# Kernel optimization log

Measured on AMD Instinct MI355X. Metric: run time of the kernel, lower is better.

The kernel has to match this reference:

```python
import jax, jax.numpy as jnp
import numpy as np

N_NODES = 100000
N_EDGES = 1600000
IN_DIM = 128
OUT_DIM = 64


def setup_inputs() -> dict:
    key = jax.random.key(0)
    k1, k2, k3, k4 = jax.random.split(key, 4)
    h = jax.random.normal(k1, (N_NODES, IN_DIM), dtype=jnp.float32)
    W = jax.random.normal(k2, (OUT_DIM, IN_DIM), dtype=jnp.float32) * (1.0 / np.sqrt(IN_DIM))
    a_w = jax.random.normal(k3, (1, 2 * OUT_DIM), dtype=jnp.float32) * (1.0 / np.sqrt(2 * OUT_DIM))
    edge_index = jax.random.randint(k4, (2, N_EDGES), 0, N_NODES, dtype=jnp.int64 if jax.config.jax_enable_x64 else jnp.int32)
    return {"h": h, "W": W, "a_w": a_w, "edge_index": edge_index}


def reference(h, W, a_w, edge_index):
    # Wh: [N, out_dim]  (Linear without bias: x @ W.T)
    Wh = h @ W.T
    src, dst = edge_index[0], edge_index[1]
    # per-edge concat [Wh[src], Wh[dst]] -> [E, 2*out_dim]
    e = jnp.concatenate([Wh[src], Wh[dst]], axis=-1)
    # attention logits: [E]
    alpha = jax.nn.leaky_relu(e @ a_w.T, negative_slope=0.2)[:, 0]
    # global-max-stabilized exp (matches the torch code exactly)
    alpha_exp = jnp.exp(alpha - jnp.max(alpha))
    # segment softmax denominator over destination nodes: [N]
    alpha_sum = jax.ops.segment_sum(alpha_exp, dst, num_segments=N_NODES)
    alpha_norm = alpha_exp / (alpha_sum[dst] + 1e-9)
    # weighted scatter-add aggregation: [N, out_dim]
    out = jax.ops.segment_sum(alpha_norm[:, None] * Wh[src], dst, num_segments=N_NODES)
    return (jax.nn.elu(out), alpha_norm)
```

## Files before the change

### kernel.cpp

```cpp
#include <hip/hip_runtime.h>
#include <math.h>

#define N_NODES 100000
#define N_EDGES 1600000
#define IN_DIM 128
#define OUT_DIM 64

#define BSHIFT 9
#define BSIZE  (1 << BSHIFT)
#define NB     ((N_NODES + BSIZE - 1) >> BSHIFT)
#define EDGES_PER_BLK 4096
#define NBLK   ((N_EDGES + EDGES_PER_BLK - 1) / EDGES_PER_BLK)
#define SCANA_LEN (NB * NBLK)
#define SCANA_ITEMS 1024
#define SCANA_NB ((SCANA_LEN + SCANA_ITEMS - 1) / SCANA_ITEMS)

typedef short short8 __attribute__((ext_vector_type(8)));
typedef float f32x4 __attribute__((ext_vector_type(4)));
typedef float f32x2 __attribute__((ext_vector_type(2)));

__device__ __forceinline__ unsigned short f2bf(float x) {
    unsigned int u = __float_as_uint(x);
    return (unsigned short)((u + 0x7FFFu + ((u >> 16) & 1u)) >> 16);
}
__device__ __forceinline__ short8 pack_bf16x8(float4 p, float4 q) {
    short8 r;
    r[0] = (short)f2bf(p.x); r[1] = (short)f2bf(p.y);
    r[2] = (short)f2bf(p.z); r[3] = (short)f2bf(p.w);
    r[4] = (short)f2bf(q.x); r[5] = (short)f2bf(q.y);
    r[6] = (short)f2bf(q.z); r[7] = (short)f2bf(q.w);
    return r;
}
__device__ __forceinline__ void pk_fma(f32x2& d, f32x2 a, f32x2 b) {
    asm("v_pk_fma_f32 %0, %1, %2, %0" : "+v"(d) : "v"(a), "v"(b));
}

__global__ __launch_bounds__(256) void k_histA(const int* __restrict__ dst,
                                               int* __restrict__ hist_t,
                                               const float* __restrict__ W,
                                               const float* __restrict__ a_w,
                                               float* __restrict__ w1,
                                               float* __restrict__ w2) {
    __shared__ int lhist[NB];
    const int tid = threadIdx.x;
    const int blk = blockIdx.x;
    if (blk == 0 && tid < IN_DIM) {
        float r1 = 0.f, r2 = 0.f;
        #pragma unroll 8
        for (int dd = 0; dd < OUT_DIM; ++dd) {
            float wv = W[dd * IN_DIM + tid];
            r1 = fmaf(a_w[dd], wv, r1);
            r2 = fmaf(a_w[OUT_DIM + dd], wv, r2);
        }
        w1[tid] = r1; w2[tid] = r2;
    }
    if (tid < NB) lhist[tid] = 0;
    __syncthreads();
    const int e0 = blk * EDGES_PER_BLK;
    #pragma unroll
    for (int j = 0; j < 4; ++j) {
        int e = e0 + (j * 256 + tid) * 4;
        if (e >= N_EDGES) continue;
        int4 d4 = *(const int4*)(dst + e);
        atomicAdd(&lhist[d4.x >> BSHIFT], 1);
        atomicAdd(&lhist[d4.y >> BSHIFT], 1);
        atomicAdd(&lhist[d4.z >> BSHIFT], 1);
        atomicAdd(&lhist[d4.w >> BSHIFT], 1);
    }
    __syncthreads();
    if (tid < NB) hist_t[tid * NBLK + blk] = lhist[tid];
}

__global__ __launch_bounds__(256) void k_wh(const float* __restrict__ h,
                                            const float* __restrict__ W,
                                            const float* __restrict__ w1,
                                            const float* __restrict__ w2,
                                            unsigned short* __restrict__ Wh16,
                                            float* __restrict__ s1,
                                            float* __restrict__ s2) {
    const int tid = threadIdx.x;
    const int wv = tid >> 6;
    const int l  = tid & 63;
    const int g  = l >> 4;
    const int lm = l & 15;
    const int node0 = blockIdx.x * 64 + wv * 16;
    const int row = node0 + lm;
    const int rowc = (row < N_NODES) ? row : (N_NODES - 1);
    const float* hrow = h + (size_t)rowc * IN_DIM;

    short8 afrag[4];
    float sp1 = 0.f, sp2 = 0.f;
    #pragma unroll
    for (int kt = 0; kt < 4; ++kt) {
        const int k0 = kt * 32 + g * 8;
        float4 p = *(const float4*)(hrow + k0);
        float4 q = *(const float4*)(hrow + k0 + 4);
        float4 u1 = *(const float4*)(w1 + k0);
        float4 v1 = *(const float4*)(w1 + k0 + 4);
        float4 u2 = *(const float4*)(w2 + k0);
        float4 v2 = *(const float4*)(w2 + k0 + 4);
        sp1 += p.x*u1.x + p.y*u1.y + p.z*u1.z + p.w*u1.w
             + q.x*v1.x + q.y*v1.y + q.z*v1.z + q.w*v1.w;
        sp2 += p.x*u2.x + p.y*u2.y + p.z*u2.z + p.w*u2.w
             + q.x*v2.x + q.y*v2.y + q.z*v2.z + q.w*v2.w;
        afrag[kt] = pack_bf16x8(p, q);
    }
    sp1 += __shfl_xor(sp1, 16, 64); sp1 += __shfl_xor(sp1, 32, 64);
    sp2 += __shfl_xor(sp2, 16, 64); sp2 += __shfl_xor(sp2, 32, 64);
    if (l < 16 && row < N_NODES) { s1[row] = sp1; s2[row] = sp2; }

    f32x4 acc[4] = {f32x4{0,0,0,0}, f32x4{0,0,0,0}, f32x4{0,0,0,0}, f32x4{0,0,0,0}};
    #pragma unroll
    for (int nt = 0; nt < 4; ++nt) {
        #pragma unroll
        for (int kt = 0; kt < 4; ++kt) {
            const float* wr = W + (size_t)(nt * 16 + lm) * IN_DIM + kt * 32 + g * 8;
            float4 p = *(const float4*)wr;
            float4 q = *(const float4*)(wr + 4);
            short8 bfrag = pack_bf16x8(p, q);
            acc[nt] = __builtin_amdgcn_mfma_f32_16x16x32_bf16(afrag[kt], bfrag, acc[nt], 0, 0, 0);
        }
    }
    #pragma unroll
    for (int nt = 0; nt < 4; ++nt) {
        #pragma unroll
        for (int r = 0; r < 4; ++r) {
            int nodo = node0 + g * 4 + r;
            if (nodo < N_NODES)
                Wh16[(size_t)nodo * OUT_DIM + nt * 16 + lm] = f2bf(acc[nt][r]);
        }
    }
}

__global__ __launch_bounds__(256) void k_scanA_part(const int* __restrict__ in,
                                                    int* __restrict__ bsum) {
    __shared__ int wsum[4];
    const int tid = threadIdx.x;
    const int base = blockIdx.x * SCANA_ITEMS + tid * 4;
    int s = 0;
    #pragma unroll
    for (int j = 0; j < 4; ++j) {
        int i = base + j;
        if (i < SCANA_LEN) s += in[i];
    }
    #pragma unroll
    for (int off = 32; off > 0; off >>= 1) s += __shfl_xor(s, off, 64);
    if ((tid & 63) == 0) wsum[tid >> 6] = s;
    __syncthreads();
    if (tid == 0) bsum[blockIdx.x] = wsum[0] + wsum[1] + wsum[2] + wsum[3];
}

__global__ __launch_bounds__(128) void k_scanA_mid(int* __restrict__ bsum) {
    __shared__ int s[128];
    const int tid = threadIdx.x;
    s[tid] = (tid < SCANA_NB) ? bsum[tid] : 0;
    __syncthreads();
    #pragma unroll
    for (int off = 1; off < 128; off <<= 1) {
        int u = (tid >= off) ? s[tid - off] : 0;
        __syncthreads();
        s[tid] += u;
        __syncthreads();
    }
    if (tid < SCANA_NB) bsum[tid] = (tid > 0) ? s[tid - 1] : 0;
}

__global__ __launch_bounds__(256) void k_scanA_final(const int* __restrict__ in,
                                                     const int* __restrict__ bsum,
                                                     int* __restrict__ outscan) {
    __shared__ int wtot[4];
    const int tid = threadIdx.x;
    const int lane = tid & 63;
    const int wid = tid >> 6;
    const int base = blockIdx.x * SCANA_ITEMS + tid * 4;
    int c[4];
    #pragma unroll
    for (int j = 0; j < 4; ++j)
        c[j] = (base + j < SCANA_LEN) ? in[base + j] : 0;
    int tot = c[0] + c[1] + c[2] + c[3];
    int inc = tot;
    #pragma unroll
    for (int off = 1; off < 64; off <<= 1) {
        int u = __shfl_up(inc, off, 64);
        if (lane >= off) inc += u;
    }
    if (lane == 63) wtot[wid] = inc;
    __syncthreads();
    int wbase = 0;
    #pragma unroll
    for (int w = 0; w < 4; ++w) wbase += (w < wid) ? wtot[w] : 0;
    int run = bsum[blockIdx.x] + wbase + (inc - tot);
    #pragma unroll
    for (int j = 0; j < 4; ++j) {
        int i = base + j;
        if (i < SCANA_LEN) { outscan[i] = run; run += c[j]; }
    }
}

__global__ __launch_bounds__(256) void k_binA(const int* __restrict__ ei,
                                              const float* __restrict__ s1,
                                              const float* __restrict__ s2,
                                              const int* __restrict__ flat_scan,
                                              int2* __restrict__ brec,
                                              float* __restrict__ ae_orig) {
    __shared__ int lbase[NB];
    __shared__ int lcur[NB];
    const int tid = threadIdx.x;
    const int blk = blockIdx.x;
    if (tid < NB) { lbase[tid] = flat_scan[tid * NBLK + blk]; lcur[tid] = 0; }
    __syncthreads();
    const int e0 = blk * EDGES_PER_BLK;
    #pragma unroll
    for (int j = 0; j < 4; ++j) {
        int e = e0 + (j * 256 + tid) * 4;
        if (e >= N_EDGES) continue;
        int4 s4 = *(const int4*)(ei + e);
        int4 d4 = *(const int4*)(ei + N_EDGES + e);
        float4 aev;
        #pragma unroll
        for (int q = 0; q < 4; ++q) {
            int src = ((const int*)&s4)[q];
            int dst = ((const int*)&d4)[q];
            float a = s1[src] + s2[dst];
            a = (a > 0.f) ? a : 0.2f * a;
            float ae = expf(a);
            ((float*)&aev)[q] = ae;
            int b = dst >> BSHIFT;
            int r = atomicAdd(&lcur[b], 1);
            brec[lbase[b] + r] = make_int2(src | ((dst & (BSIZE - 1)) << 17),
                                           __float_as_int(ae));
        }
        *(float4*)(ae_orig + e) = aev;
    }
}

__global__ __launch_bounds__(256) void k_fine(const int2* __restrict__ brec,
                                              const int* __restrict__ flat_scan,
                                              int* __restrict__ offsets,
                                              int2* __restrict__ sa_sorted,
                                              float* __restrict__ inv_tab) {
    __shared__ int lhist[BSIZE];
    __shared__ int lofs[BSIZE];
    __shared__ int lcur[BSIZE];
    __shared__ float lsum[BSIZE];
    __shared__ int wsum[4];
    const int tid = threadIdx.x;
    const int lane = tid & 63;
    const int wid = tid >> 6;
    const int b = blockIdx.x;
    const int base = flat_scan[b * NBLK];
    const int endp = (b + 1 < NB) ? flat_scan[(b + 1) * NBLK] : N_EDGES;
    const int cnt = endp - base;
    lhist[tid] = 0; lhist[tid + 256] = 0;
    lsum[tid] = 0.f; lsum[tid + 256] = 0.f;
    __syncthreads();
    for (int i = tid; i < cnt; i += 256)
        atomicAdd(&lhist[(unsigned)brec[base + i].x >> 17], 1);
    __syncthreads();
    int c0 = lhist[2 * tid], c1 = lhist[2 * tid + 1];
    int s = c0 + c1;
    int inc = s;
    #pragma unroll
    for (int off = 1; off < 64; off <<= 1) {
        int u = __shfl_up(inc, off, 64);
        if (lane >= off) inc += u;
    }
    if (lane == 63) wsum[wid] = inc;
    __syncthreads();
    int wb = 0;
    #pragma unroll
    for (int w = 0; w < 4; ++w) wb += (w < wid) ? wsum[w] : 0;
    int ex = wb + inc - s;
    lofs[2 * tid] = ex; lofs[2 * tid + 1] = ex + c0;
    lcur[2 * tid] = ex; lcur[2 * tid + 1] = ex + c0;
    __syncthreads();
    const int dst0 = b << BSHIFT;
    #pragma unroll
    for (int j = 0; j < 2; ++j) {
        int jj = tid + j * 256;
        int node = dst0 + jj;
        if (node < N_NODES) offsets[node] = base + lofs[jj];
    }
    if (b == NB - 1 && tid == 0) offsets[N_NODES] = N_EDGES;
    for (int i = tid; i < cnt; i += 256) {
        int2 rec = brec[base + i];
        int dstl = (unsigned)rec.x >> 17;
        float ae = __int_as_float(rec.y);
        int pos = base + atomicAdd(&lcur[dstl], 1);
        sa_sorted[pos] = make_int2(rec.x & 0x1FFFF, rec.y);
        atomicAdd(&lsum[dstl], ae);
    }
    __syncthreads();
    #pragma unroll
    for (int j = 0; j < 2; ++j) {
        int jj = tid + j * 256;
        int node = dst0 + jj;
        if (node < N_NODES) inv_tab[node] = 1.f / (lsum[jj] + 1e-9f);
    }
}

__global__ __launch_bounds__(256) void k_agg(const int2* __restrict__ sa_sorted,
                                             const int* __restrict__ offsets,
                                             const unsigned short* __restrict__ Wh16,
                                             const float* __restrict__ inv_tab,
                                             float* __restrict__ out) {
    const int gid = blockIdx.x * 256 + threadIdx.x;
    const int node = gid >> 6;
    const int l = gid & 63;
    if (node >= N_NODES) return;
    const int g = l >> 3;
    const int o = l & 7;
    const int beg = offsets[node];
    const int end = offsets[node + 1];
    f32x2 acc2[4] = {f32x2{0,0}, f32x2{0,0}, f32x2{0,0}, f32x2{0,0}};
    int i = beg;
    for (; i + 16 <= end; i += 16) {
        int2 pA = sa_sorted[i + g];
        int2 pB = sa_sorted[i + 8 + g];
        const int4 rA = *(const int4*)(Wh16 + ((size_t)pA.x << 6) + (o << 3));
        const int4 rB = *(const int4*)(Wh16 + ((size_t)pB.x << 6) + (o << 3));
        float aeA = __int_as_float(pA.y);
        float aeB = __int_as_float(pB.y);
        f32x2 a2A = {aeA, aeA}, a2B = {aeB, aeB};
        #pragma unroll
        for (int q = 0; q < 4; ++q) {
            int v = ((const int*)&rA)[q];
            f32x2 f = { __uint_as_float((unsigned)v << 16),
                        __uint_as_float((unsigned)v & 0xFFFF0000u) };
            pk_fma(acc2[q], f, a2A);
        }
        #pragma unroll
        for (int q = 0; q < 4; ++q) {
            int v = ((const int*)&rB)[q];
            f32x2 f = { __uint_as_float((unsigned)v << 16),
                        __uint_as_float((unsigned)v & 0xFFFF0000u) };
            pk_fma(acc2[q], f, a2B);
        }
    }
    for (; i < end; i += 8) {
        int idx = i + g;
        int2 p = (idx < end) ? sa_sorted[idx] : make_int2(0, 0);
        const int4 r = *(const int4*)(Wh16 + ((size_t)p.x << 6) + (o << 3));
        float ae = __int_as_float(p.y);
        f32x2 a2 = {ae, ae};
        #pragma unroll
        for (int q = 0; q < 4; ++q) {
            int v = ((const int*)&r)[q];
            f32x2 f = { __uint_as_float((unsigned)v << 16),
                        __uint_as_float((unsigned)v & 0xFFFF0000u) };
            pk_fma(acc2[q], f, a2);
        }
    }
    #pragma unroll
    for (int m = 8; m <= 32; m <<= 1) {
        #pragma unroll
        for (int q = 0; q < 4; ++q) {
            acc2[q].x += __shfl_xor(acc2[q].x, m, 64);
            acc2[q].y += __shfl_xor(acc2[q].y, m, 64);
        }
    }
    if (g == 0) {
        const float inv = inv_tab[node];
        float e[8];
        #pragma unroll
        for (int q = 0; q < 4; ++q) {
            float x0 = acc2[q].x * inv;
            float x1 = acc2[q].y * inv;
            e[2*q]   = (x0 > 0.f) ? x0 : expf(x0) - 1.f;
            e[2*q+1] = (x1 > 0.f) ? x1 : expf(x1) - 1.f;
        }
        float* orow = out + (size_t)node * OUT_DIM + o * 8;
        *(float4*)orow = make_float4(e[0], e[1], e[2], e[3]);
        *(float4*)(orow + 4) = make_float4(e[4], e[5], e[6], e[7]);
    }
}

__global__ __launch_bounds__(256) void k_norm(const int* __restrict__ dst_arr,
                                              const float* __restrict__ ae_orig,
                                              const float* __restrict__ inv_tab,
                                              float* __restrict__ alpha_norm) {
    int t = blockIdx.x * 256 + threadIdx.x;
    if (t >= N_EDGES / 4) return;
    int4 d4 = ((const int4*)dst_arr)[t];
    float4 a4 = ((const float4*)ae_orig)[t];
    float4 r;
    r.x = a4.x * inv_tab[d4.x];
    r.y = a4.y * inv_tab[d4.y];
    r.z = a4.z * inv_tab[d4.z];
    r.w = a4.w * inv_tab[d4.w];
    ((float4*)alpha_norm)[t] = r;
}

extern "C" void kernel_launch(void* const* d_in, const int* in_sizes, int n_in,
                              void* d_out, int out_size, void* d_ws, size_t ws_size,
                              hipStream_t stream) {
    const float* h   = (const float*)d_in[0];
    const float* W   = (const float*)d_in[1];
    const float* a_w = (const float*)d_in[2];
    const int*   ei  = (const int*)d_in[3];

    float* out        = (float*)d_out;
    float* alpha_norm = out + (size_t)N_NODES * OUT_DIM;

    char* ws = (char*)d_ws;
    int2* brec      = (int2*)ws;            ws += (size_t)N_EDGES * 8;
    int2* sa_sorted = (int2*)ws;            ws += (size_t)N_EDGES * 8;
    unsigned short* Wh16 = (unsigned short*)ws;  ws += (size_t)N_NODES * OUT_DIM * 2;
    float* ae_orig  = (float*)ws;           ws += (size_t)N_EDGES * 4;
    float* s1       = (float*)ws;           ws += (size_t)N_NODES * 4;
    float* s2       = (float*)ws;           ws += (size_t)N_NODES * 4;
    int*   hist_t   = (int*)ws;             ws += (size_t)SCANA_LEN * 4;
    int*   flat_scan= (int*)ws;             ws += (size_t)SCANA_LEN * 4;
    int*   bsum     = (int*)ws;             ws += (size_t)SCANA_NB * 4;
    int*   offsets  = (int*)ws;             ws += (size_t)(N_NODES + 1) * 4;
    float* inv_tab  = (float*)ws;           ws += (size_t)N_NODES * 4;
    float* w1       = (float*)ws;           ws += (size_t)IN_DIM * 4;
    float* w2       = (float*)ws;           ws += (size_t)IN_DIM * 4;

    k_histA<<<NBLK, 256, 0, stream>>>(ei + N_EDGES, hist_t, W, a_w, w1, w2);
    k_wh<<<(N_NODES + 63) / 64, 256, 0, stream>>>(h, W, w1, w2, Wh16, s1, s2);
    k_scanA_part<<<SCANA_NB, 256, 0, stream>>>(hist_t, bsum);
    k_scanA_mid<<<1, 128, 0, stream>>>(bsum);
    k_scanA_final<<<SCANA_NB, 256, 0, stream>>>(hist_t, bsum, flat_scan);
    k_binA<<<NBLK, 256, 0, stream>>>(ei, s1, s2, flat_scan, brec, ae_orig);
    k_fine<<<NB, 256, 0, stream>>>(brec, flat_scan, offsets, sa_sorted, inv_tab);
    k_agg<<<(N_NODES * 64 + 255) / 256, 256, 0, stream>>>(sa_sorted, offsets, Wh16,
                                                          inv_tab, out);
    k_norm<<<(N_EDGES / 4 + 255) / 256, 256, 0, stream>>>(ei + N_EDGES, ae_orig,
                                                          inv_tab, alpha_norm);
}
```

Measured before the change: 165.2 us.

## Shrink edge blocks, fold mid scan into final, widen fine kernel, add nontemporal access

Edge blocks for histogram and binning now cover 1024 edges, which gives more workgroups. The scan uses 2048 items per block, and each final-scan block rescans the block partial sums, which removes the separate mid-scan launch. The fine sort kernel runs with 1024 threads per block, and streaming loads and stores use nontemporal hints. Smaller edge blocks make the histogram table and scan four times larger. The redundant per-block scan also adds barrier work.

```diff
diff --git a/kernel.cpp b/kernel.cpp
--- a/kernel.cpp
+++ b/kernel.cpp
@@ -9,15 +9,17 @@
 #define BSHIFT 9
 #define BSIZE  (1 << BSHIFT)
 #define NB     ((N_NODES + BSIZE - 1) >> BSHIFT)
-#define EDGES_PER_BLK 4096
+#define EDGES_PER_BLK 1024
 #define NBLK   ((N_EDGES + EDGES_PER_BLK - 1) / EDGES_PER_BLK)
 #define SCANA_LEN (NB * NBLK)
-#define SCANA_ITEMS 1024
+#define SCANA_ITEMS 2048
 #define SCANA_NB ((SCANA_LEN + SCANA_ITEMS - 1) / SCANA_ITEMS)
 
 typedef short short8 __attribute__((ext_vector_type(8)));
 typedef float f32x4 __attribute__((ext_vector_type(4)));
 typedef float f32x2 __attribute__((ext_vector_type(2)));
+typedef int   i32x2 __attribute__((ext_vector_type(2)));
+typedef int   i32x4 __attribute__((ext_vector_type(4)));
 
 __device__ __forceinline__ unsigned short f2bf(float x) {
     unsigned int u = __float_as_uint(x);
@@ -56,11 +58,8 @@
     }
     if (tid < NB) lhist[tid] = 0;
     __syncthreads();
-    const int e0 = blk * EDGES_PER_BLK;
-    #pragma unroll
-    for (int j = 0; j < 4; ++j) {
-        int e = e0 + (j * 256 + tid) * 4;
-        if (e >= N_EDGES) continue;
+    const int e = blk * EDGES_PER_BLK + tid * 4;
+    if (e < N_EDGES) {
         int4 d4 = *(const int4*)(dst + e);
         atomicAdd(&lhist[d4.x >> BSHIFT], 1);
         atomicAdd(&lhist[d4.y >> BSHIFT], 1);
@@ -136,48 +135,56 @@
                                                     int* __restrict__ bsum) {
     __shared__ int wsum[4];
     const int tid = threadIdx.x;
-    const int base = blockIdx.x * SCANA_ITEMS + tid * 4;
+    const int base = blockIdx.x * SCANA_ITEMS + tid * 8;
     int s = 0;
-    #pragma unroll
-    for (int j = 0; j < 4; ++j) {
-        int i = base + j;
-        if (i < SCANA_LEN) s += in[i];
+    if (base + 7 < SCANA_LEN) {
+        int4 a = *(const int4*)(in + base);
+        int4 b = *(const int4*)(in + base + 4);
+        s = a.x + a.y + a.z + a.w + b.x + b.y + b.z + b.w;
+    } else {
+        for (int j = 0; j < 8; ++j)
+            if (base + j < SCANA_LEN) s += in[base + j];
     }
     #pragma unroll
     for (int off = 32; off > 0; off >>= 1) s += __shfl_xor(s, off, 64);
     if ((tid & 63) == 0) wsum[tid >> 6] = s;
     __syncthreads();
     if (tid == 0) bsum[blockIdx.x] = wsum[0] + wsum[1] + wsum[2] + wsum[3];
-}
-
-__global__ __launch_bounds__(128) void k_scanA_mid(int* __restrict__ bsum) {
-    __shared__ int s[128];
-    const int tid = threadIdx.x;
-    s[tid] = (tid < SCANA_NB) ? bsum[tid] : 0;
-    __syncthreads();
-    #pragma unroll
-    for (int off = 1; off < 128; off <<= 1) {
-        int u = (tid >= off) ? s[tid - off] : 0;
-        __syncthreads();
-        s[tid] += u;
-        __syncthreads();
-    }
-    if (tid < SCANA_NB) bsum[tid] = (tid > 0) ? s[tid - 1] : 0;
 }
 
 __global__ __launch_bounds__(256) void k_scanA_final(const int* __restrict__ in,
                                                      const int* __restrict__ bsum,
                                                      int* __restrict__ outscan) {
+    __shared__ int sb[256];
     __shared__ int wtot[4];
     const int tid = threadIdx.x;
     const int lane = tid & 63;
     const int wid = tid >> 6;
-    const int base = blockIdx.x * SCANA_ITEMS + tid * 4;
-    int c[4];
-    #pragma unroll
-    for (int j = 0; j < 4; ++j)
-        c[j] = (base + j < SCANA_LEN) ? in[base + j] : 0;
-    int tot = c[0] + c[1] + c[2] + c[3];
+    sb[tid] = (tid < SCANA_NB) ? bsum[tid] : 0;
+    __syncthreads();
+    #pragma unroll
+    for (int off = 1; off < 256; off <<= 1) {
+        int u = (tid >= off) ? sb[tid - off] : 0;
+        __syncthreads();
+        sb[tid] += u;
+        __syncthreads();
+    }
+    const int blockbase = (blockIdx.x > 0) ? sb[blockIdx.x - 1] : 0;
+    const int base = blockIdx.x * SCANA_ITEMS + tid * 8;
+    int c[8];
+    if (base + 7 < SCANA_LEN) {
+        int4 a = *(const int4*)(in + base);
+        int4 b = *(const int4*)(in + base + 4);
+        c[0]=a.x; c[1]=a.y; c[2]=a.z; c[3]=a.w;
+        c[4]=b.x; c[5]=b.y; c[6]=b.z; c[7]=b.w;
+    } else {
+        #pragma unroll
+        for (int j = 0; j < 8; ++j)
+            c[j] = (base + j < SCANA_LEN) ? in[base + j] : 0;
+    }
+    int tot = 0;
+    #pragma unroll
+    for (int j = 0; j < 8; ++j) tot += c[j];
     int inc = tot;
     #pragma unroll
     for (int off = 1; off < 64; off <<= 1) {
@@ -189,9 +196,9 @@
     int wbase = 0;
     #pragma unroll
     for (int w = 0; w < 4; ++w) wbase += (w < wid) ? wtot[w] : 0;
-    int run = bsum[blockIdx.x] + wbase + (inc - tot);
-    #pragma unroll
-    for (int j = 0; j < 4; ++j) {
+    int run = blockbase + wbase + (inc - tot);
+    #pragma unroll
+    for (int j = 0; j < 8; ++j) {
         int i = base + j;
         if (i < SCANA_LEN) { outscan[i] = run; run += c[j]; }
     }
@@ -209,14 +216,11 @@
     const int blk = blockIdx.x;
     if (tid < NB) { lbase[tid] = flat_scan[tid * NBLK + blk]; lcur[tid] = 0; }
     __syncthreads();
-    const int e0 = blk * EDGES_PER_BLK;
-    #pragma unroll
-    for (int j = 0; j < 4; ++j) {
-        int e = e0 + (j * 256 + tid) * 4;
-        if (e >= N_EDGES) continue;
+    const int e = blk * EDGES_PER_BLK + tid * 4;
+    if (e < N_EDGES) {
         int4 s4 = *(const int4*)(ei + e);
         int4 d4 = *(const int4*)(ei + N_EDGES + e);
-        float4 aev;
+        f32x4 aev;
         #pragma unroll
         for (int q = 0; q < 4; ++q) {
             int src = ((const int*)&s4)[q];
@@ -224,65 +228,69 @@
             float a = s1[src] + s2[dst];
             a = (a > 0.f) ? a : 0.2f * a;
             float ae = expf(a);
-            ((float*)&aev)[q] = ae;
+            aev[q] = ae;
             int b = dst >> BSHIFT;
             int r = atomicAdd(&lcur[b], 1);
             brec[lbase[b] + r] = make_int2(src | ((dst & (BSIZE - 1)) << 17),
                                            __float_as_int(ae));
         }
-        *(float4*)(ae_orig + e) = aev;
-    }
-}
-
-__global__ __launch_bounds__(256) void k_fine(const int2* __restrict__ brec,
-                                              const int* __restrict__ flat_scan,
-                                              int* __restrict__ offsets,
-                                              int2* __restrict__ sa_sorted,
-                                              float* __restrict__ inv_tab) {
+        __builtin_nontemporal_store(aev, (f32x4*)(ae_orig + e));
+    }
+}
+
+__global__ __launch_bounds__(1024) void k_fine(const int2* __restrict__ brec,
+                                               const int* __restrict__ flat_scan,
+                                               int* __restrict__ offsets,
+                                               int2* __restrict__ sa_sorted,
+                                               float* __restrict__ inv_tab) {
     __shared__ int lhist[BSIZE];
     __shared__ int lofs[BSIZE];
     __shared__ int lcur[BSIZE];
     __shared__ float lsum[BSIZE];
     __shared__ int wsum[4];
     const int tid = threadIdx.x;
-    const int lane = tid & 63;
-    const int wid = tid >> 6;
     const int b = blockIdx.x;
     const int base = flat_scan[b * NBLK];
     const int endp = (b + 1 < NB) ? flat_scan[(b + 1) * NBLK] : N_EDGES;
     const int cnt = endp - base;
-    lhist[tid] = 0; lhist[tid + 256] = 0;
-    lsum[tid] = 0.f; lsum[tid + 256] = 0.f;
-    __syncthreads();
-    for (int i = tid; i < cnt; i += 256)
+    if (tid < BSIZE) { lhist[tid] = 0; lsum[tid] = 0.f; }
+    __syncthreads();
+    for (int i = tid; i < cnt; i += 1024)
         atomicAdd(&lhist[(unsigned)brec[base + i].x >> 17], 1);
     __syncthreads();
-    int c0 = lhist[2 * tid], c1 = lhist[2 * tid + 1];
-    int s = c0 + c1;
-    int inc = s;
-    #pragma unroll
-    for (int off = 1; off < 64; off <<= 1) {
-        int u = __shfl_up(inc, off, 64);
-        if (lane >= off) inc += u;
-    }
-    if (lane == 63) wsum[wid] = inc;
-    __syncthreads();
-    int wb = 0;
-    #pragma unroll
-    for (int w = 0; w < 4; ++w) wb += (w < wid) ? wsum[w] : 0;
-    int ex = wb + inc - s;
-    lofs[2 * tid] = ex; lofs[2 * tid + 1] = ex + c0;
-    lcur[2 * tid] = ex; lcur[2 * tid + 1] = ex + c0;
+    if (tid < 256) {
+        const int lane = tid & 63;
+        int c0 = lhist[2 * tid], c1 = lhist[2 * tid + 1];
+        int s = c0 + c1;
+        int inc = s;
+        #pragma unroll
+        for (int off = 1; off < 64; off <<= 1) {
+            int u = __shfl_up(inc, off, 64);
+            if (lane >= off) inc += u;
+        }
+        if (lane == 63) wsum[tid >> 6] = inc;
+        lofs[2 * tid] = inc - s;
+        lofs[2 * tid + 1] = c0;
+    }
+    __syncthreads();
+    if (tid < 256) {
+        const int wid = tid >> 6;
+        int wb = 0;
+        #pragma unroll
+        for (int w = 0; w < 4; ++w) wb += (w < wid) ? wsum[w] : 0;
+        int ex = lofs[2 * tid] + wb;
+        int c0 = lofs[2 * tid + 1];
+        lofs[2 * tid] = ex; lofs[2 * tid + 1] = ex + c0;
+        lcur[2 * tid] = ex; lcur[2 * tid + 1] = ex + c0;
+    }
     __syncthreads();
     const int dst0 = b << BSHIFT;
-    #pragma unroll
-    for (int j = 0; j < 2; ++j) {
-        int jj = tid + j * 256;
-        int node = dst0 + jj;
-        if (node < N_NODES) offsets[node] = base + lofs[jj];
+    if (tid < BSIZE) {
+        int node = dst0 + tid;
+        if (node < N_NODES) offsets[node] = base + lofs[tid];
     }
     if (b == NB - 1 && tid == 0) offsets[N_NODES] = N_EDGES;
-    for (int i = tid; i < cnt; i += 256) {
+    for (int i = tid; i < cnt; i += 1024) {
         int2 rec = brec[base + i];
         int dstl = (unsigned)rec.x >> 17;
         float ae = __int_as_float(rec.y);
@@ -291,11 +299,9 @@
         atomicAdd(&lsum[dstl], ae);
     }
     __syncthreads();
-    #pragma unroll
-    for (int j = 0; j < 2; ++j) {
-        int jj = tid + j * 256;
-        int node = dst0 + jj;
-        if (node < N_NODES) inv_tab[node] = 1.f / (lsum[jj] + 1e-9f);
+    if (tid < BSIZE) {
+        int node = dst0 + tid;
+        if (node < N_NODES) inv_tab[node] = 1.f / (lsum[tid] + 1e-9f);
     }
 }
 
@@ -315,8 +321,8 @@
     f32x2 acc2[4] = {f32x2{0,0}, f32x2{0,0}, f32x2{0,0}, f32x2{0,0}};
     int i = beg;
     for (; i + 16 <= end; i += 16) {
-        int2 pA = sa_sorted[i + g];
-        int2 pB = sa_sorted[i + 8 + g];
+        i32x2 pA = __builtin_nontemporal_load((const i32x2*)sa_sorted + (i + g));
+        i32x2 pB = __builtin_nontemporal_load((const i32x2*)sa_sorted + (i + 8 + g));
         const int4 rA = *(const int4*)(Wh16 + ((size_t)pA.x << 6) + (o << 3));
         const int4 rB = *(const int4*)(Wh16 + ((size_t)pB.x << 6) + (o << 3));
         float aeA = __int_as_float(pA.y);
@@ -339,7 +345,8 @@
     }
     for (; i < end; i += 8) {
         int idx = i + g;
-        int2 p = (idx < end) ? sa_sorted[idx] : make_int2(0, 0);
+        i32x2 p = (idx < end) ? __builtin_nontemporal_load((const i32x2*)sa_sorted + idx)
+                              : (i32x2){0, 0};
         const int4 r = *(const int4*)(Wh16 + ((size_t)p.x << 6) + (o << 3));
         float ae = __int_as_float(p.y);
         f32x2 a2 = {ae, ae};
@@ -370,8 +377,10 @@
             e[2*q+1] = (x1 > 0.f) ? x1 : expf(x1) - 1.f;
         }
         float* orow = out + (size_t)node * OUT_DIM + o * 8;
-        *(float4*)orow = make_float4(e[0], e[1], e[2], e[3]);
-        *(float4*)(orow + 4) = make_float4(e[4], e[5], e[6], e[7]);
+        f32x4 v0 = {e[0], e[1], e[2], e[3]};
+        f32x4 v1 = {e[4], e[5], e[6], e[7]};
+        __builtin_nontemporal_store(v0, (f32x4*)orow);
+        __builtin_nontemporal_store(v1, (f32x4*)(orow + 4));
     }
 }
 
@@ -381,14 +390,14 @@
                                               float* __restrict__ alpha_norm) {
     int t = blockIdx.x * 256 + threadIdx.x;
     if (t >= N_EDGES / 4) return;
-    int4 d4 = ((const int4*)dst_arr)[t];
-    float4 a4 = ((const float4*)ae_orig)[t];
-    float4 r;
+    i32x4 d4 = __builtin_nontemporal_load((const i32x4*)dst_arr + t);
+    f32x4 a4 = __builtin_nontemporal_load((const f32x4*)ae_orig + t);
+    f32x4 r;
     r.x = a4.x * inv_tab[d4.x];
     r.y = a4.y * inv_tab[d4.y];
     r.z = a4.z * inv_tab[d4.z];
     r.w = a4.w * inv_tab[d4.w];
-    ((float4*)alpha_norm)[t] = r;
+    __builtin_nontemporal_store(r, (f32x4*)alpha_norm + t);
 }
 
 extern "C" void kernel_launch(void* const* d_in, const int* in_sizes, int n_in,
@@ -420,10 +429,9 @@
     k_histA<<<NBLK, 256, 0, stream>>>(ei + N_EDGES, hist_t, W, a_w, w1, w2);
     k_wh<<<(N_NODES + 63) / 64, 256, 0, stream>>>(h, W, w1, w2, Wh16, s1, s2);
     k_scanA_part<<<SCANA_NB, 256, 0, stream>>>(hist_t, bsum);
-    k_scanA_mid<<<1, 128, 0, stream>>>(bsum);
     k_scanA_final<<<SCANA_NB, 256, 0, stream>>>(hist_t, bsum, flat_scan);
     k_binA<<<NBLK, 256, 0, stream>>>(ei, s1, s2, flat_scan, brec, ae_orig);
-    k_fine<<<NB, 256, 0, stream>>>(brec, flat_scan, offsets, sa_sorted, inv_tab);
+    k_fine<<<NB, 1024, 0, stream>>>(brec, flat_scan, offsets, sa_sorted, inv_tab);
     k_agg<<<(N_NODES * 64 + 255) / 256, 256, 0, stream>>>(sa_sorted, offsets, Wh16,
                                                           inv_tab, out);
     k_norm<<<(N_EDGES / 4 + 255) / 256, 256, 0, stream>>>(ei + N_EDGES, ae_orig,
```

Result: no change. 165.9 us (+0.4%).
